# Kernel tuning notes

Measured on AMD Instinct MI355X. Metric: run time of the kernel, lower is better.

## Reference

```python
import jax, jax.numpy as jnp
import numpy as np

B, T, N = 16, 1024, 4096
A, C = 16, 128           # n_areas, n_channels_per_region
N_PER = N // A           # 256 neurons per area (halfbin_X = 0)


def setup_inputs() -> dict:
    key = jax.random.key(0)
    kx, kw, kb = jax.random.split(key, 3)
    x = jax.random.normal(kx, (B, T, N), dtype=jnp.float32)
    # region label per neuron: sorted, equal counts per area (matches area_ind_list_list)
    neuron_regions = (jnp.arange(N) // N_PER).astype(jnp.int64)
    is_left = jnp.ones((N,), dtype=bool)  # accepted but unused, as in source
    # stacked per-area nn.Linear params: W[a] is [C, n_per], b[a] is [C]
    W = jax.random.normal(kw, (A, C, N_PER), dtype=jnp.float32) * 0.02
    b = jax.random.normal(kb, (A, C), dtype=jnp.float32) * 0.02
    return {"x": x, "W": W, "b": b, "neuron_regions": neuron_regions, "is_left": is_left}


def reference(x, W, b, neuron_regions, is_left):
    # Gather neurons by region (stable sort of region labels -> contiguous area blocks),
    # apply per-area linear over the neuron axis, scatter into output slices.
    Bb, Tt, Nn = x.shape
    Aa, Cc, nper = W.shape
    order = jnp.argsort(neuron_regions)            # gather: neurons grouped by area
    xg = x[:, :, order].reshape(Bb, Tt, Aa, nper)  # [B,T,A,n_per]
    emb = jnp.einsum('btan,acn->btac', xg, W) + b  # per-area Linear, [B,T,A,C]
    emb = emb.reshape(Bb, Tt, Aa * Cc)
    # output is width A*C*2; second half is never written (stays zero) per source
    out = jnp.concatenate([emb, jnp.zeros_like(emb)], axis=-1)  # [B,T,2*A*C]
    return out
```

## Files before the change

kernel.cpp:

```cpp
#include <hip/hip_runtime.h>
#include <hip/hip_bf16.h>


typedef __attribute__((ext_vector_type(8))) short bf16x8;
typedef __attribute__((ext_vector_type(16))) float f32x16;

static constexpr int NX   = 4096;
static constexpr int OW   = 4096;
static constexpr int KDIM = 256;
static constexpr int CCH  = 128;

__global__ __launch_bounds__(256)
void prep_w(const float* __restrict__ W, __hip_bfloat16* __restrict__ P) {
    const int t = blockIdx.x * 256 + threadIdx.x;
    for (int s = t; s < 65536; s += 16384) {
        const int a  = s >> 12;
        const int w  = s & 4095;
        const int ks = w >> 8;
        const int n  = (w >> 6) & 3;
        const int l  = w & 63;
        const int ch = n * 32 + (l & 31);
        const int k0 = ks * 16 + (l >> 5) * 8;
        const float* src = W + ((long)a * CCH + ch) * KDIM + k0;
        const float4 w0 = *(const float4*)(src);
        const float4 w1 = *(const float4*)(src + 4);
        union { bf16x8 v; __hip_bfloat162 h[4]; } pw;
        pw.h[0] = __float22bfloat162_rn(make_float2(w0.x, w0.y));
        pw.h[1] = __float22bfloat162_rn(make_float2(w0.z, w0.w));
        pw.h[2] = __float22bfloat162_rn(make_float2(w1.x, w1.y));
        pw.h[3] = __float22bfloat162_rn(make_float2(w1.z, w1.w));
        *(bf16x8*)((char*)P + ((long)s << 4)) = pw.v;
    }
}

__global__ __launch_bounds__(256, 6)
void stitch_kernel(const float* __restrict__ x,
                   const __hip_bfloat16* __restrict__ Pw,
                   const float* __restrict__ bias,
                   float* __restrict__ out) {
    const int tid  = threadIdx.x;
    const int lane = tid & 63;
    const int wid  = tid >> 6;
    const int bid  = blockIdx.x;
    const int area = bid & 15;
    const int rowbase = (bid >> 4) * 32;

    __shared__ char As[32 * 512];

    float4 sv[8];
    const float* xb = x + (long)rowbase * NX + area * KDIM + (lane << 2);
#pragma unroll
    for (int i = 0; i < 8; ++i)
        sv[i] = *(const float4*)(xb + (long)(wid + (i << 2)) * NX);

    {
        float4* o4 = (float4*)out + 512 + area * (CCH / 4);
        const float4 z = {0.f, 0.f, 0.f, 0.f};
#pragma unroll
        for (int i = 0; i < 4; ++i) {
            const int idx = i * 256 + tid;
            const int r = idx >> 5, g = idx & 31;
            o4[(long)(rowbase + r) * (OW / 4) + g] = z;
        }
    }

    const int slotl   = lane >> 1;
    const int halfoff = (lane & 1) << 3;
#pragma unroll
    for (int i = 0; i < 8; ++i) {
        const int r = wid + (i << 2);
        union { unsigned long long u; __hip_bfloat162 h[2]; } pw;
        pw.h[0] = __float22bfloat162_rn(make_float2(sv[i].x, sv[i].y));
        pw.h[1] = __float22bfloat162_rn(make_float2(sv[i].z, sv[i].w));
        *(unsigned long long*)(&As[(r << 9) + ((slotl ^ (r & 7)) << 4) + halfoff]) = pw.u;
    }
    __syncthreads();

    const int row = lane & 31;
    const int kh  = lane >> 5;
    const bf16x8* bpa = (const bf16x8*)Pw + (long)area * 4096 + wid * 64 + lane;

    f32x16 acc;
#pragma unroll
    for (int r = 0; r < 16; ++r) acc[r] = 0.f;

#pragma unroll
    for (int ks = 0; ks < 16; ++ks) {
        const int slot = (ks << 1) + kh;
        const bf16x8 af = *(const bf16x8*)(&As[(row << 9) + ((slot ^ (row & 7)) << 4)]);
        const bf16x8 bf = bpa[ks << 8];
        acc = __builtin_amdgcn_mfma_f32_32x32x16_bf16(af, bf, acc, 0, 0, 0);
    }

    const int gcol = area * CCH + wid * 32 + row;
    const float bv = bias[gcol];
    const long rb = rowbase + 4 * kh;
#pragma unroll
    for (int r = 0; r < 16; ++r) {
        const long grow = rb + (r & 3) + ((r >> 2) << 3);
        out[grow * OW + gcol] = acc[r] + bv;
    }
}

extern "C" void kernel_launch(void* const* d_in, const int* in_sizes, int n_in,
                              void* d_out, int out_size, void* d_ws, size_t ws_size,
                              hipStream_t stream) {
    const float* x    = (const float*)d_in[0];
    const float* W    = (const float*)d_in[1];
    const float* bias = (const float*)d_in[2];
    float* out = (float*)d_out;
    __hip_bfloat16* P = (__hip_bfloat16*)d_ws;

    prep_w<<<64, 256, 0, stream>>>(W, P);
    stitch_kernel<<<8192, 256, 0, stream>>>(x, P, bias, out);
}
```

Baseline: 112.8 us.

## Use nontemporal loads/stores, split x staging into two halves, raise occupancy

The streaming reads of x and the writes of output and zero padding now use nontemporal builtins so they do not pollute the caches. The x tile is staged into LDS in two halves of four rows each, which reduces live registers and allows launch bounds to request 8 waves instead of 6. prep_w also drops its strided loop and launches one thread per element with 256 blocks. The trade-off is less load-level parallelism per thread, since the second half of the loads is serialized after the first half's conversion.

```diff
diff --git a/kernel.cpp b/kernel.cpp
--- a/kernel.cpp
+++ b/kernel.cpp
@@ -4,6 +4,7 @@
 
 typedef __attribute__((ext_vector_type(8))) short bf16x8;
 typedef __attribute__((ext_vector_type(16))) float f32x16;
+typedef __attribute__((ext_vector_type(4)))  float f32x4;
 
 static constexpr int NX   = 4096;
 static constexpr int OW   = 4096;
@@ -12,28 +13,26 @@
 
 __global__ __launch_bounds__(256)
 void prep_w(const float* __restrict__ W, __hip_bfloat16* __restrict__ P) {
-    const int t = blockIdx.x * 256 + threadIdx.x;
-    for (int s = t; s < 65536; s += 16384) {
-        const int a  = s >> 12;
-        const int w  = s & 4095;
-        const int ks = w >> 8;
-        const int n  = (w >> 6) & 3;
-        const int l  = w & 63;
-        const int ch = n * 32 + (l & 31);
-        const int k0 = ks * 16 + (l >> 5) * 8;
-        const float* src = W + ((long)a * CCH + ch) * KDIM + k0;
-        const float4 w0 = *(const float4*)(src);
-        const float4 w1 = *(const float4*)(src + 4);
-        union { bf16x8 v; __hip_bfloat162 h[4]; } pw;
-        pw.h[0] = __float22bfloat162_rn(make_float2(w0.x, w0.y));
-        pw.h[1] = __float22bfloat162_rn(make_float2(w0.z, w0.w));
-        pw.h[2] = __float22bfloat162_rn(make_float2(w1.x, w1.y));
-        pw.h[3] = __float22bfloat162_rn(make_float2(w1.z, w1.w));
-        *(bf16x8*)((char*)P + ((long)s << 4)) = pw.v;
-    }
+    const int s = blockIdx.x * 256 + threadIdx.x;
+    const int a  = s >> 12;
+    const int w  = s & 4095;
+    const int ks = w >> 8;
+    const int n  = (w >> 6) & 3;
+    const int l  = w & 63;
+    const int ch = n * 32 + (l & 31);
+    const int k0 = ks * 16 + (l >> 5) * 8;
+    const float* src = W + ((long)a * CCH + ch) * KDIM + k0;
+    const f32x4 w0 = *(const f32x4*)(src);
+    const f32x4 w1 = *(const f32x4*)(src + 4);
+    union { bf16x8 v; __hip_bfloat162 h[4]; } pw;
+    pw.h[0] = __float22bfloat162_rn(make_float2(w0.x, w0.y));
+    pw.h[1] = __float22bfloat162_rn(make_float2(w0.z, w0.w));
+    pw.h[2] = __float22bfloat162_rn(make_float2(w1.x, w1.y));
+    pw.h[3] = __float22bfloat162_rn(make_float2(w1.z, w1.w));
+    *(bf16x8*)((char*)P + ((long)s << 4)) = pw.v;
 }
 
-__global__ __launch_bounds__(256, 6)
+__global__ __launch_bounds__(256, 8)
 void stitch_kernel(const float* __restrict__ x,
                    const __hip_bfloat16* __restrict__ Pw,
                    const float* __restrict__ bias,
@@ -47,28 +46,43 @@
 
     __shared__ char As[32 * 512];
 
-    float4 sv[8];
     const float* xb = x + (long)rowbase * NX + area * KDIM + (lane << 2);
+    const int slotl   = lane >> 1;
+    const int halfoff = (lane & 1) << 3;
+
+    f32x4 sv[4];
 #pragma unroll
-    for (int i = 0; i < 8; ++i)
-        sv[i] = *(const float4*)(xb + (long)(wid + (i << 2)) * NX);
+    for (int i = 0; i < 4; ++i)
+        sv[i] = __builtin_nontemporal_load(
+            (const f32x4*)(xb + (long)(wid + (i << 2)) * NX));
 
     {
-        float4* o4 = (float4*)out + 512 + area * (CCH / 4);
-        const float4 z = {0.f, 0.f, 0.f, 0.f};
+        f32x4* o4 = (f32x4*)out + 512 + area * (CCH / 4);
+        const f32x4 z = {0.f, 0.f, 0.f, 0.f};
 #pragma unroll
         for (int i = 0; i < 4; ++i) {
             const int idx = i * 256 + tid;
             const int r = idx >> 5, g = idx & 31;
-            o4[(long)(rowbase + r) * (OW / 4) + g] = z;
+            __builtin_nontemporal_store(z, o4 + (long)(rowbase + r) * (OW / 4) + g);
         }
     }
 
-    const int slotl   = lane >> 1;
-    const int halfoff = (lane & 1) << 3;
 #pragma unroll
-    for (int i = 0; i < 8; ++i) {
+    for (int i = 0; i < 4; ++i) {
         const int r = wid + (i << 2);
+        union { unsigned long long u; __hip_bfloat162 h[2]; } pw;
+        pw.h[0] = __float22bfloat162_rn(make_float2(sv[i].x, sv[i].y));
+        pw.h[1] = __float22bfloat162_rn(make_float2(sv[i].z, sv[i].w));
+        *(unsigned long long*)(&As[(r << 9) + ((slotl ^ (r & 7)) << 4) + halfoff]) = pw.u;
+    }
+
+#pragma unroll
+    for (int i = 0; i < 4; ++i)
+        sv[i] = __builtin_nontemporal_load(
+            (const f32x4*)(xb + (long)(wid + 16 + (i << 2)) * NX));
+#pragma unroll
+    for (int i = 0; i < 4; ++i) {
+        const int r = wid + 16 + (i << 2);
         union { unsigned long long u; __hip_bfloat162 h[2]; } pw;
         pw.h[0] = __float22bfloat162_rn(make_float2(sv[i].x, sv[i].y));
         pw.h[1] = __float22bfloat162_rn(make_float2(sv[i].z, sv[i].w));
@@ -98,7 +112,7 @@
 #pragma unroll
     for (int r = 0; r < 16; ++r) {
         const long grow = rb + (r & 3) + ((r >> 2) << 3);
-        out[grow * OW + gcol] = acc[r] + bv;
+        __builtin_nontemporal_store(acc[r] + bv, out + grow * OW + gcol);
     }
 }
 
@@ -111,6 +125,6 @@
     float* out = (float*)d_out;
     __hip_bfloat16* P = (__hip_bfloat16*)d_ws;
 
-    prep_w<<<64, 256, 0, stream>>>(W, P);
+    prep_w<<<256, 256, 0, stream>>>(W, P);
     stitch_kernel<<<8192, 256, 0, stream>>>(x, P, bias, out);
 }
```

Result: faster. 110.0 us (-2.5%).
